# Kernel tuning notes

Hardware: AMD Instinct MI355X
Metric: run time of the kernel (lower is better)

Reference implementation:

```python
import jax, jax.numpy as jnp
import numpy as np

B, S, I, H = 64, 256, 512, 512


def setup_inputs() -> dict:
    key = jax.random.key(0)
    ks = jax.random.split(key, 17)
    s = 1.0 / np.sqrt(I + H)  # torch nn.Linear default init bound

    def w(k):
        return jax.random.uniform(k, (I + H, H), jnp.float32, -s, s)

    def b(k):
        return jax.random.uniform(k, (H,), jnp.float32, -s, s)

    return {
        "x": jax.random.normal(ks[0], (B, S, I), jnp.float32),
        "Wi_f": w(ks[1]), "bi_f": b(ks[2]),
        "Wf_f": w(ks[3]), "bf_f": b(ks[4]),
        "Wc_f": w(ks[5]), "bc_f": b(ks[6]),
        "Wo_f": w(ks[7]), "bo_f": b(ks[8]),
        "Wi_b": w(ks[9]), "bi_b": b(ks[10]),
        "Wf_b": w(ks[11]), "bf_b": b(ks[12]),
        "Wc_b": w(ks[13]), "bc_b": b(ks[14]),
        "Wo_b": w(ks[15]), "bo_b": b(ks[16]),
    }


def _lstm_scan(x_sbi, Wi, bi, Wf, bf, Wc, bc, Wo, bo):
    # x_sbi: (S, B, I). Dropout is identity (eval mode).
    bsz = x_sbi.shape[1]
    hdim = Wi.shape[1]

    def step(carry, xt):
        h, c = carry
        comb = jnp.concatenate([xt, h], axis=1)  # (B, I+H)
        i_t = jax.nn.sigmoid(comb @ Wi + bi)
        f_t = jax.nn.sigmoid(comb @ Wf + bf)
        o_t = jax.nn.sigmoid(comb @ Wo + bo)
        g_t = jnp.tanh(comb @ Wc + bc)
        c_t = f_t * c + i_t * g_t
        h_t = o_t * jnp.tanh(c_t)
        return (h_t, c_t), h_t

    h0 = jnp.zeros((bsz, hdim), x_sbi.dtype)
    (_, _), hs = jax.lax.scan(step, (h0, h0), x_sbi)
    return hs  # (S, B, H)


def reference(x, Wi_f, bi_f, Wf_f, bf_f, Wc_f, bc_f, Wo_f, bo_f,
              Wi_b, bi_b, Wf_b, bf_b, Wc_b, bc_b, Wo_b, bo_b):
    xs = jnp.swapaxes(x, 0, 1)  # (S, B, I)
    fwd = _lstm_scan(xs, Wi_f, bi_f, Wf_f, bf_f, Wc_f, bc_f, Wo_f, bo_f)
    bwd = _lstm_scan(xs[::-1], Wi_b, bi_b, Wf_b, bf_b, Wc_b, bc_b, Wo_b, bo_b)[::-1]
    out = jnp.concatenate([fwd, bwd], axis=2)  # (S, B, 2H)
    return jnp.swapaxes(out, 0, 1)  # (B, S, 2H)
```

## Files before the change

### kernel.cpp

```cpp
#include <hip/hip_runtime.h>


typedef float    f32x4 __attribute__((ext_vector_type(4)));
typedef _Float16 half8 __attribute__((ext_vector_type(8)));
typedef unsigned long long u64;

#define NB 64
#define NS 256
#define NI 512
#define NH 512

__device__ inline f32x4 zero4() { f32x4 v; v[0]=0.f; v[1]=0.f; v[2]=0.f; v[3]=0.f; return v; }


__global__ void conv_x(const float* __restrict__ x, _Float16* __restrict__ xb) {
    const int i = blockIdx.x * 256 + threadIdx.x;
    const float4 a = ((const float4*)x)[2*i];
    const float4 b = ((const float4*)x)[2*i+1];
    half8 o;
    o[0]=(_Float16)a.x; o[1]=(_Float16)a.y; o[2]=(_Float16)a.z; o[3]=(_Float16)a.w;
    o[4]=(_Float16)b.x; o[5]=(_Float16)b.y; o[6]=(_Float16)b.z; o[7]=(_Float16)b.w;
    ((half8*)xb)[i] = o;
}

__global__ void pack_w(const float* __restrict__ Wi_f, const float* __restrict__ Wf_f,
                       const float* __restrict__ Wo_f, const float* __restrict__ Wc_f,
                       const float* __restrict__ Wi_b, const float* __restrict__ Wf_b,
                       const float* __restrict__ Wo_b, const float* __restrict__ Wc_b,
                       _Float16* __restrict__ WP) {
    const int idx = blockIdx.x * 256 + threadIdx.x;
    const int l  = idx & 63;
    const int g  = (idx >> 6) & 3;
    const int kk = (idx >> 8) & 15;
    const int p  = (idx >> 12) & 1;
    const int s  = (idx >> 13) & 31;
    const int d  = (idx >> 18) & 1;
    const float* W;
    if (d == 0) W = (g==0) ? Wi_f : (g==1) ? Wf_f : (g==2) ? Wo_f : Wc_f;
    else        W = (g==0) ? Wi_b : (g==1) ? Wf_b : (g==2) ? Wo_b : Wc_b;
    const int r0 = p*512 + kk*32 + (l >> 4)*8;
    const int c  = s*16 + (l & 15);
    half8 v;
    #pragma unroll
    for (int j = 0; j < 8; ++j) v[j] = (_Float16)W[(size_t)(r0 + j)*NH + c];
    *(half8*)(WP + (size_t)idx*8) = v;
}

__global__ void pack_bias(const float* __restrict__ bi_f, const float* __restrict__ bf_f,
                          const float* __restrict__ bo_f, const float* __restrict__ bc_f,
                          const float* __restrict__ bi_b, const float* __restrict__ bf_b,
                          const float* __restrict__ bo_b, const float* __restrict__ bc_b,
                          float* __restrict__ biasP) {
    const int i = blockIdx.x * 256 + threadIdx.x;
    const int c = i & 511, g = (i >> 9) & 3, d = (i >> 11) & 1;
    const float* b;
    if (d == 0) b = (g==0) ? bi_f : (g==1) ? bf_f : (g==2) ? bo_f : bc_f;
    else        b = (g==0) ? bi_b : (g==1) ? bf_b : (g==2) ? bo_b : bc_b;
    biasP[i] = b[c];
}


__global__ __launch_bounds__(256) void lstm_scan(
    const _Float16* __restrict__ xb,
    const _Float16* __restrict__ WP,
    const float*    __restrict__ biasP,
    unsigned*       __restrict__ hfrag,
    unsigned*       __restrict__ flags,
    float*          __restrict__ out)
{
    __shared__ char  ldsw[131072];
    __shared__ float redb[4][4][4][64];

    const int wg  = blockIdx.x;
    const int g8  = wg & 7;
    const int s   = wg >> 3;
    const int d   = g8 >> 2;
    const int bg  = g8 & 3;
    const int tid = threadIdx.x;
    const int w   = tid >> 6;
    const int l   = tid & 63;

    {
        const uint4* src = (const uint4*)(WP + (size_t)(d*32 + s)*65536);
        uint4* dst = (uint4*)ldsw;
        #pragma unroll
        for (int i = 0; i < 32; ++i) dst[tid + i*256] = src[tid + i*256];
    }
    __syncthreads();

    const int row_local = (l >> 4)*4 + w;
    const int col_local = l & 15;
    const int colg      = s*16 + col_local;
    const float bias0 = biasP[(d*4 + 0)*512 + colg];
    const float bias1 = biasP[(d*4 + 1)*512 + colg];
    const float bias2 = biasP[(d*4 + 2)*512 + colg];
    const float bias3 = biasP[(d*4 + 3)*512 + colg];
    float cstv = 0.f;

    const int myoff = (colg >> 5)*512 + ((colg >> 2) & 1)*256
                    + (((colg >> 3) & 3)*16 + row_local)*4 + (colg & 3);
    unsigned* grpfrag = hfrag + (size_t)g8 * 16384;
    unsigned* myflag  = flags + (size_t)(g8*32 + s) * 32;
    unsigned* pollp   = flags + (size_t)(g8*32 + w*8 + (l & 7)) * 32;

    f32x4 acc[4];
    #pragma unroll
    for (int g = 0; g < 4; ++g) acc[g] = zero4();

    bool dead = false;

    const int arow = bg*16 + (l & 15);
    const int kof  = (l >> 4) * 8;
    const int kk0  = w * 4;

    for (int t = 0; t < NS; ++t) {
        const int u = d ? (NS - 1 - t) : t;

        const _Float16* xp = xb + ((size_t)arow*NS + u)*NI + kof;
        half8 af[4];
        #pragma unroll
        for (int c = 0; c < 4; ++c) af[c] = *(const half8*)(xp + (kk0 + c)*32);
        #pragma unroll
        for (int c = 0; c < 4; ++c) {
            #pragma unroll
            for (int g = 0; g < 4; ++g) {
                const half8 b = *(const half8*)(ldsw + ((((kk0 + c)*4 + g) << 10) | (l << 4)));
                acc[g] = __builtin_amdgcn_mfma_f32_16x16x32_f16(af[c], b, acc[g], 0, 0, 0);
            }
        }

        if (t > 0) {
            const unsigned tagv = (unsigned)t;
            const unsigned tgt4 = 4u * (unsigned)t;

            if (!dead) {
                unsigned v = 0xFFFFFFFFu;
                int guard = 0;
                for (;;) {
                    if (l < 8) v = __hip_atomic_load(pollp, __ATOMIC_RELAXED,
                                                     __HIP_MEMORY_SCOPE_AGENT);
                    if (!__any(v < tgt4)) break;
                    if (++guard > (1 << 18)) { dead = true; break; }
                }
            }

            const unsigned* gb = grpfrag + (size_t)(t & 1)*8192;
            u64 q[16];
            {
                int guard = 0;
                for (;;) {
                    unsigned bad = 0;
                    #pragma unroll
                    for (int c = 0; c < 4; ++c) {
                        const unsigned* blk = gb + (kk0 + c)*512;
                        const u64* p0 = (const u64*)(blk + l*4);
                        const u64* p1 = (const u64*)(blk + 256 + l*4);
                        q[c*4+0] = __hip_atomic_load(p0,     __ATOMIC_RELAXED, __HIP_MEMORY_SCOPE_AGENT);
                        q[c*4+1] = __hip_atomic_load(p0 + 1, __ATOMIC_RELAXED, __HIP_MEMORY_SCOPE_AGENT);
                        q[c*4+2] = __hip_atomic_load(p1,     __ATOMIC_RELAXED, __HIP_MEMORY_SCOPE_AGENT);
                        q[c*4+3] = __hip_atomic_load(p1 + 1, __ATOMIC_RELAXED, __HIP_MEMORY_SCOPE_AGENT);
                        #pragma unroll
                        for (int j = 0; j < 4; ++j) {
                            const u64 v = q[c*4 + j];
                            bad |= (((unsigned)(v >> 16) & 0xFFFFu) ^ tagv);
                            bad |= (((unsigned)(v >> 48))           ^ tagv);
                        }
                    }
                    if (!__any(bad != 0)) break;
                    if (dead || ++guard > (1 << 16)) { dead = true; break; }
                    __builtin_amdgcn_s_sleep(1);
                }
            }
            #pragma unroll
            for (int c = 0; c < 4; ++c) {
                union { unsigned uu[4]; half8 h; } hu;
                #pragma unroll
                for (int j = 0; j < 4; ++j) {
                    const u64 v = q[c*4 + j];
                    hu.uu[j] = ((unsigned)v & 0xFFFFu) | (((unsigned)(v >> 32)) << 16);
                }
                const half8 ah = hu.h;
                #pragma unroll
                for (int g = 0; g < 4; ++g) {
                    const half8 b = *(const half8*)(ldsw + ((((16 + kk0 + c)*4 + g) << 10) | (l << 4)));
                    acc[g] = __builtin_amdgcn_mfma_f32_16x16x32_f16(ah, b, acc[g], 0, 0, 0);
                }
            }
        }

        __syncthreads();
        #pragma unroll
        for (int g = 0; g < 4; ++g) {
            #pragma unroll
            for (int r = 0; r < 4; ++r) redb[w][g][r][l] = acc[g][r];
        }
        __syncthreads();
        {
            float s0 = 0.f, s1 = 0.f, s2 = 0.f, s3 = 0.f;
            #pragma unroll
            for (int wv = 0; wv < 4; ++wv) {
                s0 += redb[wv][0][w][l];
                s1 += redb[wv][1][w][l];
                s2 += redb[wv][2][w][l];
                s3 += redb[wv][3][w][l];
            }
            const float ig = 1.f / (1.f + __expf(-(s0 + bias0)));
            const float fg = 1.f / (1.f + __expf(-(s1 + bias1)));
            const float og = 1.f / (1.f + __expf(-(s2 + bias2)));
            const float gv = s3 + bias3;
            const float gg = 1.f - 2.f / (__expf(2.f*gv) + 1.f);
            cstv = fg*cstv + ig*gg;
            const float hvv = og * (1.f - 2.f / (__expf(2.f*cstv) + 1.f));

            const unsigned short hb = __builtin_bit_cast(unsigned short, (_Float16)hvv);
            const unsigned word = ((unsigned)(t + 1) << 16) | (unsigned)hb;
            __hip_atomic_store(grpfrag + (size_t)((t + 1) & 1)*8192 + myoff, word,
                               __ATOMIC_RELAXED, __HIP_MEMORY_SCOPE_AGENT);
            if (l == 0)
                (void)__hip_atomic_fetch_add(myflag, 1u, __ATOMIC_RELAXED,
                                             __HIP_MEMORY_SCOPE_AGENT);
            out[((size_t)(bg*16 + row_local)*NS + u)*1024 + (d << 9) + colg] = hvv;
        }
        #pragma unroll
        for (int g = 0; g < 4; ++g) acc[g] = zero4();
    }
}


extern "C" void kernel_launch(void* const* d_in, const int* in_sizes, int n_in,
                              void* d_out, int out_size, void* d_ws, size_t ws_size,
                              hipStream_t stream) {
    const float* x = (const float*)d_in[0];
    char* ws = (char*)d_ws;
    _Float16* xb    = (_Float16*)ws;
    _Float16* WP    = (_Float16*)(ws + (16u << 20));
    float*    biasP = (float*)(ws + (24u << 20));
    unsigned* hfrag = (unsigned*)(ws + (24u << 20) + (64u << 10));
    unsigned* flags = (unsigned*)(ws + (24u << 20) + (64u << 10) + (512u << 10));

    hipMemsetAsync(hfrag, 0, (512u << 10) + (32u << 10), stream);
    conv_x<<<4096, 256, 0, stream>>>(x, xb);
    pack_w<<<2048, 256, 0, stream>>>(
        (const float*)d_in[1],  (const float*)d_in[3],  (const float*)d_in[7],  (const float*)d_in[5],
        (const float*)d_in[9],  (const float*)d_in[11], (const float*)d_in[15], (const float*)d_in[13], WP);
    pack_bias<<<16, 256, 0, stream>>>(
        (const float*)d_in[2],  (const float*)d_in[4],  (const float*)d_in[8],  (const float*)d_in[6],
        (const float*)d_in[10], (const float*)d_in[12], (const float*)d_in[16], (const float*)d_in[14], biasP);
    lstm_scan<<<256, 256, 0, stream>>>(xb, WP, biasP, hfrag, flags, (float*)d_out);
}
```

Measured before the change: 798.7 us.

## Drop flag counters, poll tagged h fragments directly, prefetch next x

Removes the per-workgroup atomic flag counters and their polling loop, and relies only on the step tags embedded in each h fragment word for cross-workgroup synchronisation. The h fragment loads are issued before the input MFMAs, and on a retry only the words that are not yet valid are reloaded. The x fragments for the next timestep are prefetched one iteration ahead. This removes one global atomic round trip per step from the critical path, at the cost of extra registers and spinning directly on the data buffer.

```diff
diff --git a/kernel.cpp b/kernel.cpp
--- a/kernel.cpp
+++ b/kernel.cpp
@@ -65,7 +65,6 @@
     const _Float16* __restrict__ WP,
     const float*    __restrict__ biasP,
     unsigned*       __restrict__ hfrag,
-    unsigned*       __restrict__ flags,
     float*          __restrict__ out)
 {
     __shared__ char  ldsw[131072];
@@ -100,8 +99,6 @@
     const int myoff = (colg >> 5)*512 + ((colg >> 2) & 1)*256
                     + (((colg >> 3) & 3)*16 + row_local)*4 + (colg & 3);
     unsigned* grpfrag = hfrag + (size_t)g8 * 16384;
-    unsigned* myflag  = flags + (size_t)(g8*32 + s) * 32;
-    unsigned* pollp   = flags + (size_t)(g8*32 + w*8 + (l & 7)) * 32;
 
     f32x4 acc[4];
     #pragma unroll
@@ -113,13 +110,41 @@
     const int kof  = (l >> 4) * 8;
     const int kk0  = w * 4;
 
+    half8 af[4];
+    {
+        const int u0 = d ? (NS - 1) : 0;
+        const _Float16* xp = xb + ((size_t)arow*NS + u0)*NI + kof;
+        #pragma unroll
+        for (int c = 0; c < 4; ++c) af[c] = *(const half8*)(xp + (kk0 + c)*32);
+    }
+
     for (int t = 0; t < NS; ++t) {
         const int u = d ? (NS - 1 - t) : t;
 
-        const _Float16* xp = xb + ((size_t)arow*NS + u)*NI + kof;
-        half8 af[4];
-        #pragma unroll
-        for (int c = 0; c < 4; ++c) af[c] = *(const half8*)(xp + (kk0 + c)*32);
+        const unsigned tagv = (unsigned)t;
+        const unsigned* gb = grpfrag + (size_t)(t & 1)*8192;
+        u64 q[16];
+        if (t > 0) {
+            #pragma unroll
+            for (int c = 0; c < 4; ++c) {
+                const unsigned* blk = gb + (kk0 + c)*512;
+                const u64* p0 = (const u64*)(blk + l*4);
+                const u64* p1 = (const u64*)(blk + 256 + l*4);
+                q[c*4+0] = __hip_atomic_load(p0,     __ATOMIC_RELAXED, __HIP_MEMORY_SCOPE_AGENT);
+                q[c*4+1] = __hip_atomic_load(p0 + 1, __ATOMIC_RELAXED, __HIP_MEMORY_SCOPE_AGENT);
+                q[c*4+2] = __hip_atomic_load(p1,     __ATOMIC_RELAXED, __HIP_MEMORY_SCOPE_AGENT);
+                q[c*4+3] = __hip_atomic_load(p1 + 1, __ATOMIC_RELAXED, __HIP_MEMORY_SCOPE_AGENT);
+            }
+        }
+
+        half8 afn[4];
+        if (t + 1 < NS) {
+            const int un = d ? (NS - 2 - t) : (t + 1);
+            const _Float16* xpn = xb + ((size_t)arow*NS + un)*NI + kof;
+            #pragma unroll
+            for (int c = 0; c < 4; ++c) afn[c] = *(const half8*)(xpn + (kk0 + c)*32);
+        }
+
         #pragma unroll
         for (int c = 0; c < 4; ++c) {
             #pragma unroll
@@ -130,45 +155,31 @@
         }
 
         if (t > 0) {
-            const unsigned tagv = (unsigned)t;
-            const unsigned tgt4 = 4u * (unsigned)t;
-
-            if (!dead) {
-                unsigned v = 0xFFFFFFFFu;
-                int guard = 0;
-                for (;;) {
-                    if (l < 8) v = __hip_atomic_load(pollp, __ATOMIC_RELAXED,
-                                                     __HIP_MEMORY_SCOPE_AGENT);
-                    if (!__any(v < tgt4)) break;
-                    if (++guard > (1 << 18)) { dead = true; break; }
-                }
-            }
-
-            const unsigned* gb = grpfrag + (size_t)(t & 1)*8192;
-            u64 q[16];
-            {
-                int guard = 0;
-                for (;;) {
-                    unsigned bad = 0;
+            unsigned inv;
+            int guard = 0;
+            for (;;) {
+                inv = 0;
+                #pragma unroll
+                for (int j = 0; j < 16; ++j) {
+                    const u64 v = q[j];
+                    const bool ok = (((unsigned)(v >> 16) & 0xFFFFu) == tagv) &&
+                                    (((unsigned)(v >> 48))           == tagv);
+                    inv |= ok ? 0u : (1u << j);
+                }
+                if (!__any(inv != 0)) break;
+                if (dead || ++guard > (1 << 16)) { dead = true; break; }
+                __builtin_amdgcn_s_sleep(1);
+                #pragma unroll
+                for (int c = 0; c < 4; ++c) {
+                    const unsigned* blk = gb + (kk0 + c)*512;
                     #pragma unroll
-                    for (int c = 0; c < 4; ++c) {
-                        const unsigned* blk = gb + (kk0 + c)*512;
-                        const u64* p0 = (const u64*)(blk + l*4);
-                        const u64* p1 = (const u64*)(blk + 256 + l*4);
-                        q[c*4+0] = __hip_atomic_load(p0,     __ATOMIC_RELAXED, __HIP_MEMORY_SCOPE_AGENT);
-                        q[c*4+1] = __hip_atomic_load(p0 + 1, __ATOMIC_RELAXED, __HIP_MEMORY_SCOPE_AGENT);
-                        q[c*4+2] = __hip_atomic_load(p1,     __ATOMIC_RELAXED, __HIP_MEMORY_SCOPE_AGENT);
-                        q[c*4+3] = __hip_atomic_load(p1 + 1, __ATOMIC_RELAXED, __HIP_MEMORY_SCOPE_AGENT);
-                        #pragma unroll
-                        for (int j = 0; j < 4; ++j) {
-                            const u64 v = q[c*4 + j];
-                            bad |= (((unsigned)(v >> 16) & 0xFFFFu) ^ tagv);
-                            bad |= (((unsigned)(v >> 48))           ^ tagv);
-                        }
+                    for (int sub = 0; sub < 4; ++sub) {
+                        const int j = c*4 + sub;
+                        if (inv & (1u << j))
+                            q[j] = __hip_atomic_load(
+                                (const u64*)(blk + (sub >> 1)*256 + l*4) + (sub & 1),
+                                __ATOMIC_RELAXED, __HIP_MEMORY_SCOPE_AGENT);
                     }
-                    if (!__any(bad != 0)) break;
-                    if (dead || ++guard > (1 << 16)) { dead = true; break; }
-                    __builtin_amdgcn_s_sleep(1);
                 }
             }
             #pragma unroll
@@ -216,13 +227,14 @@
             const unsigned word = ((unsigned)(t + 1) << 16) | (unsigned)hb;
             __hip_atomic_store(grpfrag + (size_t)((t + 1) & 1)*8192 + myoff, word,
                                __ATOMIC_RELAXED, __HIP_MEMORY_SCOPE_AGENT);
-            if (l == 0)
-                (void)__hip_atomic_fetch_add(myflag, 1u, __ATOMIC_RELAXED,
-                                             __HIP_MEMORY_SCOPE_AGENT);
             out[((size_t)(bg*16 + row_local)*NS + u)*1024 + (d << 9) + colg] = hvv;
         }
         #pragma unroll
         for (int g = 0; g < 4; ++g) acc[g] = zero4();
+        if (t + 1 < NS) {
+            #pragma unroll
+            for (int c = 0; c < 4; ++c) af[c] = afn[c];
+        }
     }
 }
 
@@ -236,9 +248,8 @@
     _Float16* WP    = (_Float16*)(ws + (16u << 20));
     float*    biasP = (float*)(ws + (24u << 20));
     unsigned* hfrag = (unsigned*)(ws + (24u << 20) + (64u << 10));
-    unsigned* flags = (unsigned*)(ws + (24u << 20) + (64u << 10) + (512u << 10));
-
-    hipMemsetAsync(hfrag, 0, (512u << 10) + (32u << 10), stream);
+
+    hipMemsetAsync(hfrag, 0, 512u << 10, stream);
     conv_x<<<4096, 256, 0, stream>>>(x, xb);
     pack_w<<<2048, 256, 0, stream>>>(
         (const float*)d_in[1],  (const float*)d_in[3],  (const float*)d_in[7],  (const float*)d_in[5],
@@ -246,5 +257,5 @@
     pack_bias<<<16, 256, 0, stream>>>(
         (const float*)d_in[2],  (const float*)d_in[4],  (const float*)d_in[8],  (const float*)d_in[6],
         (const float*)d_in[10], (const float*)d_in[12], (const float*)d_in[16], (const float*)d_in[14], biasP);
-    lstm_scan<<<256, 256, 0, stream>>>(xb, WP, biasP, hfrag, flags, (float*)d_out);
-}
+    lstm_scan<<<256, 256, 0, stream>>>(xb, WP, biasP, hfrag, (float*)d_out);
+}
```

After: 1.366 ms. +71.0%, slower.

## Overlap h-fragment loads with x-MFMAs, prefetch next x, double-buffer reduction

Applied to the files above, without the earlier changes.

Issues the hidden-state fragment loads before the input-projection MFMAs so their latency overlaps compute, and prefetches the next timestep's x fragment into registers. The cross-wave reduction buffer is double-buffered by timestep parity, which removes one __syncthreads per step, and each wave keeps its own diagonal partial in registers so fewer LDS writes are needed. The final step also skips publishing h. The cost is extra register pressure from holding the prefetched x and the polled values, and the correctness of dropping the barrier depends on the parity buffering.

```diff
diff --git a/kernel.cpp b/kernel.cpp
--- a/kernel.cpp
+++ b/kernel.cpp
@@ -69,7 +69,7 @@
     float*          __restrict__ out)
 {
     __shared__ char  ldsw[131072];
-    __shared__ float redb[4][4][4][64];
+    __shared__ float redb[2][4][4][3][64];
 
     const int wg  = blockIdx.x;
     const int g8  = wg & 7;
@@ -113,27 +113,24 @@
     const int kof  = (l >> 4) * 8;
     const int kk0  = w * 4;
 
+    half8 af[4];
+    {
+        const int u0 = d ? (NS - 1) : 0;
+        const _Float16* xp = xb + ((size_t)arow*NS + u0)*NI + kof;
+        #pragma unroll
+        for (int c = 0; c < 4; ++c) af[c] = *(const half8*)(xp + (kk0 + c)*32);
+    }
+
     for (int t = 0; t < NS; ++t) {
         const int u = d ? (NS - 1 - t) : t;
 
-        const _Float16* xp = xb + ((size_t)arow*NS + u)*NI + kof;
-        half8 af[4];
-        #pragma unroll
-        for (int c = 0; c < 4; ++c) af[c] = *(const half8*)(xp + (kk0 + c)*32);
-        #pragma unroll
-        for (int c = 0; c < 4; ++c) {
-            #pragma unroll
-            for (int g = 0; g < 4; ++g) {
-                const half8 b = *(const half8*)(ldsw + ((((kk0 + c)*4 + g) << 10) | (l << 4)));
-                acc[g] = __builtin_amdgcn_mfma_f32_16x16x32_f16(af[c], b, acc[g], 0, 0, 0);
-            }
-        }
+        const unsigned tagv = (unsigned)t;
+        const unsigned* gb = grpfrag + (size_t)(t & 1)*8192;
+        u64 q[16];
 
         if (t > 0) {
-            const unsigned tagv = (unsigned)t;
-            const unsigned tgt4 = 4u * (unsigned)t;
-
             if (!dead) {
+                const unsigned tgt4 = 4u * tagv;
                 unsigned v = 0xFFFFFFFFu;
                 int guard = 0;
                 for (;;) {
@@ -143,32 +140,57 @@
                     if (++guard > (1 << 18)) { dead = true; break; }
                 }
             }
-
-            const unsigned* gb = grpfrag + (size_t)(t & 1)*8192;
-            u64 q[16];
-            {
-                int guard = 0;
-                for (;;) {
-                    unsigned bad = 0;
-                    #pragma unroll
-                    for (int c = 0; c < 4; ++c) {
-                        const unsigned* blk = gb + (kk0 + c)*512;
-                        const u64* p0 = (const u64*)(blk + l*4);
-                        const u64* p1 = (const u64*)(blk + 256 + l*4);
-                        q[c*4+0] = __hip_atomic_load(p0,     __ATOMIC_RELAXED, __HIP_MEMORY_SCOPE_AGENT);
-                        q[c*4+1] = __hip_atomic_load(p0 + 1, __ATOMIC_RELAXED, __HIP_MEMORY_SCOPE_AGENT);
-                        q[c*4+2] = __hip_atomic_load(p1,     __ATOMIC_RELAXED, __HIP_MEMORY_SCOPE_AGENT);
-                        q[c*4+3] = __hip_atomic_load(p1 + 1, __ATOMIC_RELAXED, __HIP_MEMORY_SCOPE_AGENT);
-                        #pragma unroll
-                        for (int j = 0; j < 4; ++j) {
-                            const u64 v = q[c*4 + j];
-                            bad |= (((unsigned)(v >> 16) & 0xFFFFu) ^ tagv);
-                            bad |= (((unsigned)(v >> 48))           ^ tagv);
-                        }
-                    }
-                    if (!__any(bad != 0)) break;
-                    if (dead || ++guard > (1 << 16)) { dead = true; break; }
-                    __builtin_amdgcn_s_sleep(1);
+            #pragma unroll
+            for (int c = 0; c < 4; ++c) {
+                const unsigned* blk = gb + (kk0 + c)*512;
+                const u64* p0 = (const u64*)(blk + l*4);
+                const u64* p1 = (const u64*)(blk + 256 + l*4);
+                q[c*4+0] = __hip_atomic_load(p0,     __ATOMIC_RELAXED, __HIP_MEMORY_SCOPE_AGENT);
+                q[c*4+1] = __hip_atomic_load(p0 + 1, __ATOMIC_RELAXED, __HIP_MEMORY_SCOPE_AGENT);
+                q[c*4+2] = __hip_atomic_load(p1,     __ATOMIC_RELAXED, __HIP_MEMORY_SCOPE_AGENT);
+                q[c*4+3] = __hip_atomic_load(p1 + 1, __ATOMIC_RELAXED, __HIP_MEMORY_SCOPE_AGENT);
+            }
+        }
+
+        half8 afn[4];
+        if (t + 1 < NS) {
+            const int un = d ? (NS - 2 - t) : (t + 1);
+            const _Float16* xpn = xb + ((size_t)arow*NS + un)*NI + kof;
+            #pragma unroll
+            for (int c = 0; c < 4; ++c) afn[c] = *(const half8*)(xpn + (kk0 + c)*32);
+        }
+
+        #pragma unroll
+        for (int c = 0; c < 4; ++c) {
+            #pragma unroll
+            for (int g = 0; g < 4; ++g) {
+                const half8 b = *(const half8*)(ldsw + ((((kk0 + c)*4 + g) << 10) | (l << 4)));
+                acc[g] = __builtin_amdgcn_mfma_f32_16x16x32_f16(af[c], b, acc[g], 0, 0, 0);
+            }
+        }
+
+        if (t > 0) {
+            int guard = 0;
+            for (;;) {
+                unsigned bad = 0;
+                #pragma unroll
+                for (int j = 0; j < 16; ++j) {
+                    const u64 v = q[j];
+                    bad |= (((unsigned)(v >> 16) & 0xFFFFu) ^ tagv);
+                    bad |= (((unsigned)(v >> 48))           ^ tagv);
+                }
+                if (!__any(bad != 0)) break;
+                if (dead || ++guard > (1 << 16)) { dead = true; break; }
+                __builtin_amdgcn_s_sleep(1);
+                #pragma unroll
+                for (int c = 0; c < 4; ++c) {
+                    const unsigned* blk = gb + (kk0 + c)*512;
+                    const u64* p0 = (const u64*)(blk + l*4);
+                    const u64* p1 = (const u64*)(blk + 256 + l*4);
+                    q[c*4+0] = __hip_atomic_load(p0,     __ATOMIC_RELAXED, __HIP_MEMORY_SCOPE_AGENT);
+                    q[c*4+1] = __hip_atomic_load(p0 + 1, __ATOMIC_RELAXED, __HIP_MEMORY_SCOPE_AGENT);
+                    q[c*4+2] = __hip_atomic_load(p1,     __ATOMIC_RELAXED, __HIP_MEMORY_SCOPE_AGENT);
+                    q[c*4+3] = __hip_atomic_load(p1 + 1, __ATOMIC_RELAXED, __HIP_MEMORY_SCOPE_AGENT);
                 }
             }
             #pragma unroll
@@ -188,41 +210,51 @@
             }
         }
 
-        __syncthreads();
+        const int bsel = t & 1;
         #pragma unroll
         for (int g = 0; g < 4; ++g) {
             #pragma unroll
-            for (int r = 0; r < 4; ++r) redb[w][g][r][l] = acc[g][r];
+            for (int r = 0; r < 4; ++r) {
+                if (r != w) redb[bsel][w][g][r - (r > w)][l] = acc[g][r];
+            }
         }
         __syncthreads();
         {
-            float s0 = 0.f, s1 = 0.f, s2 = 0.f, s3 = 0.f;
-            #pragma unroll
-            for (int wv = 0; wv < 4; ++wv) {
-                s0 += redb[wv][0][w][l];
-                s1 += redb[wv][1][w][l];
-                s2 += redb[wv][2][w][l];
-                s3 += redb[wv][3][w][l];
-            }
-            const float ig = 1.f / (1.f + __expf(-(s0 + bias0)));
-            const float fg = 1.f / (1.f + __expf(-(s1 + bias1)));
-            const float og = 1.f / (1.f + __expf(-(s2 + bias2)));
-            const float gv = s3 + bias3;
+            float sg[4];
+            #pragma unroll
+            for (int g = 0; g < 4; ++g) {
+                float sv = acc[g][w];
+                #pragma unroll
+                for (int wv = 0; wv < 4; ++wv) {
+                    if (wv != w) sv += redb[bsel][wv][g][w - (w > wv)][l];
+                }
+                sg[g] = sv;
+            }
+            const float ig = 1.f / (1.f + __expf(-(sg[0] + bias0)));
+            const float fg = 1.f / (1.f + __expf(-(sg[1] + bias1)));
+            const float og = 1.f / (1.f + __expf(-(sg[2] + bias2)));
+            const float gv = sg[3] + bias3;
             const float gg = 1.f - 2.f / (__expf(2.f*gv) + 1.f);
             cstv = fg*cstv + ig*gg;
             const float hvv = og * (1.f - 2.f / (__expf(2.f*cstv) + 1.f));
 
-            const unsigned short hb = __builtin_bit_cast(unsigned short, (_Float16)hvv);
-            const unsigned word = ((unsigned)(t + 1) << 16) | (unsigned)hb;
-            __hip_atomic_store(grpfrag + (size_t)((t + 1) & 1)*8192 + myoff, word,
-                               __ATOMIC_RELAXED, __HIP_MEMORY_SCOPE_AGENT);
-            if (l == 0)
-                (void)__hip_atomic_fetch_add(myflag, 1u, __ATOMIC_RELAXED,
-                                             __HIP_MEMORY_SCOPE_AGENT);
+            if (t + 1 < NS) {
+                const unsigned short hb = __builtin_bit_cast(unsigned short, (_Float16)hvv);
+                const unsigned word = ((unsigned)(t + 1) << 16) | (unsigned)hb;
+                __hip_atomic_store(grpfrag + (size_t)((t + 1) & 1)*8192 + myoff, word,
+                                   __ATOMIC_RELAXED, __HIP_MEMORY_SCOPE_AGENT);
+                if (l == 0)
+                    (void)__hip_atomic_fetch_add(myflag, 1u, __ATOMIC_RELAXED,
+                                                 __HIP_MEMORY_SCOPE_AGENT);
+            }
             out[((size_t)(bg*16 + row_local)*NS + u)*1024 + (d << 9) + colg] = hvv;
         }
         #pragma unroll
         for (int g = 0; g < 4; ++g) acc[g] = zero4();
+        if (t + 1 < NS) {
+            #pragma unroll
+            for (int c = 0; c < 4; ++c) af[c] = afn[c];
+        }
     }
 }
 
```

Result: slower. 1.288 ms (+61.3%).

## Use plain cached loads for hidden-state exchange when a group shares one XCC

Applied to the files above, without the earlier changes.

At startup each workgroup reads its XCC id and uses atomics to check whether all 32 blocks of its direction/batch group landed on the same XCC. If they did, the hidden-state fragments are read with plain vector loads instead of 64-bit agent-scope atomics, and written with plain stores followed by a waitcnt. On a failed tag check the fast path reads through 16 unrelated weight lines to push the stale data out of cache, instead of sleeping. It also skips publishing h after the last step. The gain relies on the same-XCC L2 being coherent for non-atomic traffic. That holds only if the scheduler places whole groups on one XCC, and the cache-eviction trick is fragile.

```diff
diff --git a/kernel.cpp b/kernel.cpp
--- a/kernel.cpp
+++ b/kernel.cpp
@@ -70,6 +70,7 @@
 {
     __shared__ char  ldsw[131072];
     __shared__ float redb[4][4][4][64];
+    __shared__ unsigned mode_sh;
 
     const int wg  = blockIdx.x;
     const int g8  = wg & 7;
@@ -80,6 +81,24 @@
     const int w   = tid >> 6;
     const int l   = tid & 63;
 
+    unsigned* ctrl = flags + 8192;
+
+    if (tid == 0) {
+        unsigned xcc;
+        asm volatile("s_getreg_b32 %0, hwreg(HW_REG_XCC_ID)" : "=s"(xcc));
+        atomicMax(ctrl + 8 + g8, xcc);
+        atomicMin(ctrl + 16 + g8, xcc);
+        asm volatile("s_waitcnt vmcnt(0)" ::: "memory");
+        atomicAdd(ctrl + g8, 1u);
+        int gu = 0; unsigned c;
+        do {
+            c = __hip_atomic_load(ctrl + g8, __ATOMIC_RELAXED, __HIP_MEMORY_SCOPE_AGENT);
+        } while (c < 32u && ++gu < (1 << 22));
+        const unsigned mx = __hip_atomic_load(ctrl + 8 + g8,  __ATOMIC_RELAXED, __HIP_MEMORY_SCOPE_AGENT);
+        const unsigned mn = __hip_atomic_load(ctrl + 16 + g8, __ATOMIC_RELAXED, __HIP_MEMORY_SCOPE_AGENT);
+        mode_sh = (gu < (1 << 22)) && (mn == mx);
+    }
+
     {
         const uint4* src = (const uint4*)(WP + (size_t)(d*32 + s)*65536);
         uint4* dst = (uint4*)ldsw;
@@ -87,6 +106,7 @@
         for (int i = 0; i < 32; ++i) dst[tid + i*256] = src[tid + i*256];
     }
     __syncthreads();
+    const bool fast = (mode_sh != 0);
 
     const int row_local = (l >> 4)*4 + w;
     const int col_local = l & 15;
@@ -131,9 +151,11 @@
 
         if (t > 0) {
             const unsigned tagv = (unsigned)t;
-            const unsigned tgt4 = 4u * (unsigned)t;
+            const unsigned* gb = grpfrag + (size_t)(t & 1)*8192;
+            u64 q[16];
 
             if (!dead) {
+                const unsigned tgt4 = 4u * tagv;
                 unsigned v = 0xFFFFFFFFu;
                 int guard = 0;
                 for (;;) {
@@ -143,32 +165,75 @@
                     if (++guard > (1 << 18)) { dead = true; break; }
                 }
             }
-
-            const unsigned* gb = grpfrag + (size_t)(t & 1)*8192;
-            u64 q[16];
+            asm volatile("" ::: "memory");
+
+            if (fast) {
+                #pragma unroll
+                for (int c = 0; c < 4; ++c) {
+                    const unsigned* blk = gb + (kk0 + c)*512;
+                    const uint4 a  = *(const uint4*)(blk + l*4);
+                    const uint4 b2 = *(const uint4*)(blk + 256 + l*4);
+                    q[c*4+0] = ((u64)a.y  << 32) | a.x;
+                    q[c*4+1] = ((u64)a.w  << 32) | a.z;
+                    q[c*4+2] = ((u64)b2.y << 32) | b2.x;
+                    q[c*4+3] = ((u64)b2.w << 32) | b2.z;
+                }
+            } else {
+                #pragma unroll
+                for (int c = 0; c < 4; ++c) {
+                    const unsigned* blk = gb + (kk0 + c)*512;
+                    const u64* p0 = (const u64*)(blk + l*4);
+                    const u64* p1 = (const u64*)(blk + 256 + l*4);
+                    q[c*4+0] = __hip_atomic_load(p0,     __ATOMIC_RELAXED, __HIP_MEMORY_SCOPE_AGENT);
+                    q[c*4+1] = __hip_atomic_load(p0 + 1, __ATOMIC_RELAXED, __HIP_MEMORY_SCOPE_AGENT);
+                    q[c*4+2] = __hip_atomic_load(p1,     __ATOMIC_RELAXED, __HIP_MEMORY_SCOPE_AGENT);
+                    q[c*4+3] = __hip_atomic_load(p1 + 1, __ATOMIC_RELAXED, __HIP_MEMORY_SCOPE_AGENT);
+                }
+            }
+
             {
                 int guard = 0;
                 for (;;) {
                     unsigned bad = 0;
                     #pragma unroll
-                    for (int c = 0; c < 4; ++c) {
-                        const unsigned* blk = gb + (kk0 + c)*512;
-                        const u64* p0 = (const u64*)(blk + l*4);
-                        const u64* p1 = (const u64*)(blk + 256 + l*4);
-                        q[c*4+0] = __hip_atomic_load(p0,     __ATOMIC_RELAXED, __HIP_MEMORY_SCOPE_AGENT);
-                        q[c*4+1] = __hip_atomic_load(p0 + 1, __ATOMIC_RELAXED, __HIP_MEMORY_SCOPE_AGENT);
-                        q[c*4+2] = __hip_atomic_load(p1,     __ATOMIC_RELAXED, __HIP_MEMORY_SCOPE_AGENT);
-                        q[c*4+3] = __hip_atomic_load(p1 + 1, __ATOMIC_RELAXED, __HIP_MEMORY_SCOPE_AGENT);
+                    for (int j = 0; j < 16; ++j) {
+                        const u64 v = q[j];
+                        bad |= (((unsigned)(v >> 16) & 0xFFFFu) ^ tagv);
+                        bad |= (((unsigned)(v >> 48))           ^ tagv);
+                    }
+                    if (!__any(bad != 0)) break;
+                    if (dead || ++guard > (1 << 14)) { dead = true; break; }
+                    if (fast) {
+                        unsigned dum = 0;
+                        const uint4* wp4 = (const uint4*)WP;
                         #pragma unroll
-                        for (int j = 0; j < 4; ++j) {
-                            const u64 v = q[c*4 + j];
-                            bad |= (((unsigned)(v >> 16) & 0xFFFFu) ^ tagv);
-                            bad |= (((unsigned)(v >> 48))           ^ tagv);
+                        for (int i = 0; i < 16; ++i)
+                            dum += wp4[(size_t)(w*1024 + i*64 + l)].x;
+                        asm volatile("" :: "v"(dum));
+                        asm volatile("" ::: "memory");
+                        #pragma unroll
+                        for (int c = 0; c < 4; ++c) {
+                            const unsigned* blk = gb + (kk0 + c)*512;
+                            const uint4 a  = *(const uint4*)(blk + l*4);
+                            const uint4 b2 = *(const uint4*)(blk + 256 + l*4);
+                            q[c*4+0] = ((u64)a.y  << 32) | a.x;
+                            q[c*4+1] = ((u64)a.w  << 32) | a.z;
+                            q[c*4+2] = ((u64)b2.y << 32) | b2.x;
+                            q[c*4+3] = ((u64)b2.w << 32) | b2.z;
+                        }
+                    } else {
+                        __builtin_amdgcn_s_sleep(1);
+                        #pragma unroll
+                        for (int c = 0; c < 4; ++c) {
+                            const unsigned* blk = gb + (kk0 + c)*512;
+                            const u64* p0 = (const u64*)(blk + l*4);
+                            const u64* p1 = (const u64*)(blk + 256 + l*4);
+                            q[c*4+0] = __hip_atomic_load(p0,     __ATOMIC_RELAXED, __HIP_MEMORY_SCOPE_AGENT);
+                            q[c*4+1] = __hip_atomic_load(p0 + 1, __ATOMIC_RELAXED, __HIP_MEMORY_SCOPE_AGENT);
+                            q[c*4+2] = __hip_atomic_load(p1,     __ATOMIC_RELAXED, __HIP_MEMORY_SCOPE_AGENT);
+                            q[c*4+3] = __hip_atomic_load(p1 + 1, __ATOMIC_RELAXED, __HIP_MEMORY_SCOPE_AGENT);
                         }
                     }
-                    if (!__any(bad != 0)) break;
-                    if (dead || ++guard > (1 << 16)) { dead = true; break; }
-                    __builtin_amdgcn_s_sleep(1);
                 }
             }
             #pragma unroll
@@ -212,13 +277,23 @@
             cstv = fg*cstv + ig*gg;
             const float hvv = og * (1.f - 2.f / (__expf(2.f*cstv) + 1.f));
 
-            const unsigned short hb = __builtin_bit_cast(unsigned short, (_Float16)hvv);
-            const unsigned word = ((unsigned)(t + 1) << 16) | (unsigned)hb;
-            __hip_atomic_store(grpfrag + (size_t)((t + 1) & 1)*8192 + myoff, word,
-                               __ATOMIC_RELAXED, __HIP_MEMORY_SCOPE_AGENT);
-            if (l == 0)
-                (void)__hip_atomic_fetch_add(myflag, 1u, __ATOMIC_RELAXED,
-                                             __HIP_MEMORY_SCOPE_AGENT);
+            if (t + 1 < NS) {
+                const unsigned short hb = __builtin_bit_cast(unsigned short, (_Float16)hvv);
+                const unsigned word = ((unsigned)(t + 1) << 16) | (unsigned)hb;
+                unsigned* dst = grpfrag + (size_t)((t + 1) & 1)*8192 + myoff;
+                if (fast) {
+                    *dst = word;
+                    asm volatile("s_waitcnt vmcnt(0)" ::: "memory");
+                    if (l == 0)
+                        (void)__hip_atomic_fetch_add(myflag, 1u, __ATOMIC_RELAXED,
+                                                     __HIP_MEMORY_SCOPE_AGENT);
+                } else {
+                    __hip_atomic_store(dst, word, __ATOMIC_RELAXED, __HIP_MEMORY_SCOPE_AGENT);
+                    if (l == 0)
+                        (void)__hip_atomic_fetch_add(myflag, 1u, __ATOMIC_RELAXED,
+                                                     __HIP_MEMORY_SCOPE_AGENT);
+                }
+            }
             out[((size_t)(bg*16 + row_local)*NS + u)*1024 + (d << 9) + colg] = hvv;
         }
         #pragma unroll
@@ -238,7 +313,8 @@
     unsigned* hfrag = (unsigned*)(ws + (24u << 20) + (64u << 10));
     unsigned* flags = (unsigned*)(ws + (24u << 20) + (64u << 10) + (512u << 10));
 
-    hipMemsetAsync(hfrag, 0, (512u << 10) + (32u << 10), stream);
+    hipMemsetAsync(hfrag, 0, (512u << 10) + (32u << 10) + 64u, stream);
+    hipMemsetAsync((char*)flags + (32u << 10) + 64u, 0xFF, 32u, stream);
     conv_x<<<4096, 256, 0, stream>>>(x, xb);
     pack_w<<<2048, 256, 0, stream>>>(
         (const float*)d_in[1],  (const float*)d_in[3],  (const float*)d_in[7],  (const float*)d_in[5],
```

New measurement: 763.0 us, median of 3. 1.05x faster.
